# Kernel tuning notes

Measured on AMD Instinct MI355X. Metric: run time of the kernel, lower is better.

Reference implementation:

```python
import jax, jax.numpy as jnp
import numpy as np

B, L, HID = 4, 4096, 1024
H, D = 16, 64  # num_heads, head_dim


def setup_inputs() -> dict:
    key = jax.random.key(0)
    ks = jax.random.split(key, 5)
    s = 1.0 / np.sqrt(HID)
    mk = lambda k: jax.random.uniform(k, (HID, HID), minval=-s, maxval=s, dtype=jnp.float32)
    return {
        "x": jax.random.normal(ks[0], (B, L, HID), dtype=jnp.float32),
        "Wq": mk(ks[1]), "bq": jnp.zeros((HID,), jnp.float32),
        "Wk": mk(ks[2]), "bk": jnp.zeros((HID,), jnp.float32),
        "Wv": mk(ks[3]), "bv": jnp.zeros((HID,), jnp.float32),
        "Wo": mk(ks[4]), "bo": jnp.zeros((HID,), jnp.float32),
    }


def reference(x, Wq, bq, Wk, bk, Wv, bv, Wo, bo):
    Bx, Lx, _ = x.shape
    # projections (weights stored [in, out])
    q = (x @ Wq + bq).reshape(Bx, Lx, H, D)
    k = (x @ Wk + bk).reshape(Bx, Lx, H, D)
    v = (x @ Wv + bv).reshape(Bx, Lx, H, D)
    # Single window (L <= window_size): torch matmul batches over (B, L) and
    # contracts head_dim -> per-token head-to-head scores [B, L, H, H].
    scores = jnp.einsum('blhd,bled->blhe', q, k) / np.sqrt(D).astype(np.float32)
    probs = jax.nn.softmax(scores, axis=-1)
    out = jnp.einsum('blhe,bled->blhd', probs, v).reshape(Bx, Lx, HID)
    return out @ Wo + bo
```

## Files before the change

### kernel.cpp

```cpp
#include <hip/hip_runtime.h>
#include <stdint.h>


typedef __attribute__((ext_vector_type(8))) short short8;
typedef __attribute__((ext_vector_type(4))) float floatx4;
typedef __attribute__((address_space(1))) unsigned int gu32;
typedef __attribute__((address_space(3))) unsigned int lu32;

#define HID 1024
#define MTOK 16384
#define WELEM (HID * HID)
#define XELEM (MTOK * HID)

#define SBAR() __builtin_amdgcn_s_barrier()
#define WAITLGKM() do { asm volatile("s_waitcnt lgkmcnt(0)" ::: "memory"); \
                        __builtin_amdgcn_sched_barrier(0); } while (0)
#define VMCNT(n) do { asm volatile("s_waitcnt vmcnt(" #n ")" ::: "memory"); \
                      __builtin_amdgcn_sched_barrier(0); } while (0)

__device__ __forceinline__ unsigned short f2bf(float f) {
  union { float f; uint32_t u; } v; v.f = f;
  uint32_t u = v.u;
  u += 0x7fffu + ((u >> 16) & 1u);
  return (unsigned short)(u >> 16);
}

__global__ __launch_bounds__(256) void cvt_x_kernel(const float* __restrict__ x,
                                                    unsigned short* __restrict__ xb) {
  const int idx = blockIdx.x * 256 + threadIdx.x;
  float4 v = ((const float4*)x)[idx];
  ushort4 o;
  o.x = f2bf(v.x); o.y = f2bf(v.y); o.z = f2bf(v.z); o.w = f2bf(v.w);
  ((ushort4*)xb)[idx] = o;
}

__global__ __launch_bounds__(256) void cvt_w_kernel(const float* __restrict__ W0,
                                                    const float* __restrict__ W1,
                                                    const float* __restrict__ W2,
                                                    const float* __restrict__ W3,
                                                    unsigned short* __restrict__ WT) {
  const float* W = (blockIdx.z == 0) ? W0 : (blockIdx.z == 1) ? W1
                   : (blockIdx.z == 2) ? W2 : W3;
  unsigned short* out = WT + (size_t)blockIdx.z * WELEM;
  __shared__ float tile[64][65];
  const int t = threadIdx.x;
  const int n0 = blockIdx.x * 64, k0 = blockIdx.y * 64;
#pragma unroll
  for (int i = 0; i < 4; i++) {
    const int row = i * 16 + (t >> 4);
    const int col = (t & 15) * 4;
    float4 v = *(const float4*)&W[(size_t)(k0 + row) * HID + n0 + col];
    tile[row][col] = v.x; tile[row][col + 1] = v.y;
    tile[row][col + 2] = v.z; tile[row][col + 3] = v.w;
  }
  __syncthreads();
#pragma unroll
  for (int i = 0; i < 4; i++) {
    const int n = i * 16 + (t >> 4);
    const int k = (t & 15) * 4;
    ushort4 o;
    o.x = f2bf(tile[k][n]);     o.y = f2bf(tile[k + 1][n]);
    o.z = f2bf(tile[k + 2][n]); o.w = f2bf(tile[k + 3][n]);
    *(ushort4*)&out[(size_t)(n0 + n) * HID + k0 + k] = o;
  }
}

template <bool QKV>
__global__ __launch_bounds__(512, 2) void gemm256(
    const unsigned short* __restrict__ A,
    const unsigned short* __restrict__ BTb,
    const float* __restrict__ b0, const float* __restrict__ b1,
    const float* __restrict__ b2,
    void* __restrict__ Cv)
{
  __shared__ short8 smem_[131072 / 16];
  char* smem = (char*)smem_;

  constexpr int R = QKV ? 3 : 1;
  const int bid = blockIdx.x;
  const int xcd = bid & 7;
  const int j = bid >> 3;
  const int nb0 = j >> 3;
  const int mb = xcd * 8 + (j & 7);
  const int m0 = mb * 256;
  const int cb = nb0 * 256;

  const unsigned short* BT0 = QKV ? BTb : (BTb + (size_t)3 * WELEM);

  const int t_ = threadIdx.x;
  const int wv = t_ >> 6, lane = t_ & 63;
  const int quad = lane >> 4, r16 = lane & 15;
  const int wm = wv >> 2, wn = wv & 3;

  const int srow = wv * 16 + (lane >> 2);
  const int scol = ((lane & 3) ^ ((lane >> 3) & 3)) * 8;
  const unsigned short* Ag = A + (size_t)(m0 + srow) * HID + scol;
  const unsigned short* Bg = BT0 + (size_t)(cb + srow) * HID + scol;

  const int qsw = (quad ^ ((r16 >> 1) & 3)) << 4;
  const char* Ard = smem + wm * 16384 + r16 * 64 + qsw;
  const char* Brd = smem + 32768 + (wn >> 1) * 16384 + ((wn & 1) * 64 + r16) * 64 + qsw;

  floatx4 acc[8][4] = {};

  auto stageA = [&](int h, int tt) {
    const unsigned short* s = Ag + (size_t)h * 128 * HID + tt * 64;
    char* d = smem + ((tt & 1) << 16) + h * 16384 + wv * 1024;
    __builtin_amdgcn_global_load_lds((const gu32*)s,        (lu32*)d,          16, 0, 0);
    __builtin_amdgcn_global_load_lds((const gu32*)(s + 32), (lu32*)(d + 8192), 16, 0, 0);
  };
  auto stageB = [&](int h, int tt) {
    const unsigned short* s = Bg + (size_t)h * 128 * HID + tt * 64;
    char* d = smem + ((tt & 1) << 16) + 32768 + h * 16384 + wv * 1024;
    __builtin_amdgcn_global_load_lds((const gu32*)s,        (lu32*)d,          16, 0, 0);
    __builtin_amdgcn_global_load_lds((const gu32*)(s + 32), (lu32*)(d + 8192), 16, 0, 0);
  };

  const int NT = HID / 64;

  short8 alo[4][2], ahi[4][2];
  short8 b01[2][2], b23[2][2];

  stageA(0, 0); stageA(1, 0); stageB(0, 0); stageB(1, 0);
  VMCNT(0);
  SBAR();

  for (int r = 0; r < R; ++r) {
    for (int t = 0; t < NT; ++t) {
      const int bufb = (t & 1) << 16;
      const bool more = (t + 1 < NT);

      if (more) { stageA(0, t + 1); stageA(1, t + 1);
                  stageB(0, t + 1); stageB(1, t + 1); }

#pragma unroll
      for (int ks = 0; ks < 2; ++ks)
#pragma unroll
        for (int mi = 0; mi < 4; ++mi)
          alo[mi][ks] = *(const short8*)(Ard + bufb + ks * 8192 + mi * 1024);
#pragma unroll
      for (int ks = 0; ks < 2; ++ks)
#pragma unroll
        for (int ni = 0; ni < 2; ++ni)
          b01[ni][ks] = *(const short8*)(Brd + bufb + ks * 8192 + ni * 1024);
#pragma unroll
      for (int ks = 0; ks < 2; ++ks)
#pragma unroll
        for (int ni = 0; ni < 2; ++ni)
          b23[ni][ks] = *(const short8*)(Brd + bufb + ks * 8192 + (2 + ni) * 1024);
#pragma unroll
      for (int ks = 0; ks < 2; ++ks)
#pragma unroll
        for (int mi = 0; mi < 4; ++mi)
          ahi[mi][ks] = *(const short8*)(Ard + bufb + ks * 8192 + (4 + mi) * 1024);

      __builtin_amdgcn_s_setprio(1);
#pragma unroll
      for (int ks = 0; ks < 2; ++ks)
#pragma unroll
        for (int mi = 0; mi < 4; ++mi)
#pragma unroll
          for (int ni = 0; ni < 2; ++ni)
            acc[mi][ni] = __builtin_amdgcn_mfma_f32_16x16x32_bf16(alo[mi][ks], b01[ni][ks], acc[mi][ni], 0, 0, 0);
#pragma unroll
      for (int ks = 0; ks < 2; ++ks)
#pragma unroll
        for (int mi = 0; mi < 4; ++mi)
#pragma unroll
          for (int ni = 0; ni < 2; ++ni)
            acc[mi][2 + ni] = __builtin_amdgcn_mfma_f32_16x16x32_bf16(alo[mi][ks], b23[ni][ks], acc[mi][2 + ni], 0, 0, 0);
#pragma unroll
      for (int ks = 0; ks < 2; ++ks)
#pragma unroll
        for (int mi = 0; mi < 4; ++mi)
#pragma unroll
          for (int ni = 0; ni < 2; ++ni)
            acc[4 + mi][2 + ni] = __builtin_amdgcn_mfma_f32_16x16x32_bf16(ahi[mi][ks], b23[ni][ks], acc[4 + mi][2 + ni], 0, 0, 0);
#pragma unroll
      for (int ks = 0; ks < 2; ++ks)
#pragma unroll
        for (int mi = 0; mi < 4; ++mi)
#pragma unroll
          for (int ni = 0; ni < 2; ++ni)
            acc[4 + mi][ni] = __builtin_amdgcn_mfma_f32_16x16x32_bf16(ahi[mi][ks], b01[ni][ks], acc[4 + mi][ni], 0, 0, 0);
      __builtin_amdgcn_s_setprio(0);

      WAITLGKM();
      VMCNT(0);
      SBAR();
    }

    if (r + 1 < R) {
      Bg += WELEM;
      stageA(0, 0); stageA(1, 0); stageB(0, 0); stageB(1, 0);
    }

    {
      const float* bias = QKV ? ((r == 0) ? b0 : ((r == 1) ? b1 : b2)) : b0;
      float bvv[4];
#pragma unroll
      for (int ni = 0; ni < 4; ++ni) bvv[ni] = bias[cb + wn * 64 + ni * 16 + r16];

      const int row0 = m0 + wm * 128 + quad * 4;
      unsigned short* outb = (unsigned short*)Cv + (size_t)r * XELEM;
      float* outf = (float*)Cv;
#pragma unroll
      for (int mi = 0; mi < 8; ++mi) {
#pragma unroll
        for (int rr = 0; rr < 4; ++rr) {
          const size_t roff = (size_t)(row0 + mi * 16 + rr) * HID + cb + wn * 64 + r16;
#pragma unroll
          for (int ni = 0; ni < 4; ++ni) {
            const float val = acc[mi][ni][rr] + bvv[ni];
            if constexpr (QKV) outb[roff + ni * 16] = f2bf(val);
            else               outf[roff + ni * 16] = val;
          }
        }
      }
    }

    if (r + 1 < R) {
#pragma unroll
      for (int mi = 0; mi < 8; ++mi)
#pragma unroll
        for (int ni = 0; ni < 4; ++ni)
          acc[mi][ni] = floatx4{0.f, 0.f, 0.f, 0.f};
      VMCNT(0);
      SBAR();
    }
  }
}

__global__ __launch_bounds__(256) void attn_kernel(const unsigned short* qkv,
                                                   unsigned short* attn) {
  __shared__ unsigned short vls[4][1056];
  __shared__ unsigned short pls[4][16 * 24];

  const int t = threadIdx.x;
  const int wv = t >> 6, lane = t & 63;
  const int quad = lane >> 4, r16 = lane & 15;
  const size_t base = ((size_t)blockIdx.x * 4 + wv) * HID;
  const unsigned short* qp = qkv + base;
  const unsigned short* kp = qkv + (size_t)XELEM + base;
  const unsigned short* vp = qkv + 2 * (size_t)XELEM + base;

  __builtin_amdgcn_global_load_lds((const gu32*)(vp + lane * 8),       (lu32*)&vls[wv][0],   16, 0, 0);
  __builtin_amdgcn_global_load_lds((const gu32*)(vp + 512 + lane * 8), (lu32*)&vls[wv][528], 16, 0, 0);

  short8 qf0 = *(const short8*)(qp + r16 * 64 + quad * 8);
  short8 qf1 = *(const short8*)(qp + r16 * 64 + quad * 8 + 32);
  short8 kf0 = *(const short8*)(kp + r16 * 64 + quad * 8);
  short8 kf1 = *(const short8*)(kp + r16 * 64 + quad * 8 + 32);

  floatx4 sc = {0.f, 0.f, 0.f, 0.f};
  sc = __builtin_amdgcn_mfma_f32_16x16x32_bf16(qf0, kf0, sc, 0, 0, 0);
  sc = __builtin_amdgcn_mfma_f32_16x16x32_bf16(qf1, kf1, sc, 0, 0, 0);

#pragma unroll
  for (int rr = 0; rr < 4; rr++) {
    float s = sc[rr] * 0.125f;
    float m = s;
#pragma unroll
    for (int off = 1; off < 16; off <<= 1) m = fmaxf(m, __shfl_xor(m, off));
    float ex = __expf(s - m);
    float sum = ex;
#pragma unroll
    for (int off = 1; off < 16; off <<= 1) sum += __shfl_xor(sum, off);
    pls[wv][(quad * 4 + rr) * 24 + r16] = f2bf(ex / sum);
  }

  __syncthreads();

  const short8 zero8 = {0, 0, 0, 0, 0, 0, 0, 0};
  short8 af = zero8;
  short8 bf[4] = {zero8, zero8, zero8, zero8};
  if (quad < 2) {
    af = *(const short8*)&pls[wv][r16 * 24 + quad * 8];
#pragma unroll
    for (int c = 0; c < 4; c++)
#pragma unroll
      for (int jj = 0; jj < 8; jj++)
        bf[c][jj] = (short)vls[wv][quad * 528 + jj * 64 + c * 16 + r16];
  }

  floatx4 ov[4];
#pragma unroll
  for (int c = 0; c < 4; c++) {
    floatx4 z = {0.f, 0.f, 0.f, 0.f};
    ov[c] = __builtin_amdgcn_mfma_f32_16x16x32_bf16(af, bf[c], z, 0, 0, 0);
  }

#pragma unroll
  for (int rr = 0; rr < 4; rr++)
#pragma unroll
    for (int c = 0; c < 4; c++)
      attn[base + (size_t)(quad * 4 + rr) * 64 + c * 16 + r16] = f2bf(ov[c][rr]);
}

extern "C" void kernel_launch(void* const* d_in, const int* in_sizes, int n_in,
                              void* d_out, int out_size, void* d_ws, size_t ws_size,
                              hipStream_t stream) {
  const float* x  = (const float*)d_in[0];
  const float* Wq = (const float*)d_in[1];
  const float* bq = (const float*)d_in[2];
  const float* Wk = (const float*)d_in[3];
  const float* bk = (const float*)d_in[4];
  const float* Wv = (const float*)d_in[5];
  const float* bv = (const float*)d_in[6];
  const float* Wo = (const float*)d_in[7];
  const float* bo = (const float*)d_in[8];

  char* ws = (char*)d_ws;
  unsigned short* xb  = (unsigned short*)ws;
  unsigned short* wt  = (unsigned short*)(ws + (size_t)XELEM * 2);
  unsigned short* qkv = wt + 4 * (size_t)WELEM;

  cvt_x_kernel<<<XELEM / 1024, 256, 0, stream>>>(x, xb);
  cvt_w_kernel<<<dim3(16, 16, 4), 256, 0, stream>>>(Wq, Wk, Wv, Wo, wt);
  gemm256<true><<<256, 512, 0, stream>>>(xb, wt, bq, bk, bv, (void*)qkv);
  attn_kernel<<<4096, 256, 0, stream>>>(qkv, qkv);
  gemm256<false><<<256, 512, 0, stream>>>(qkv, wt, bo, bo, bo, d_out);
}
```

Measured before the change: 296.3 us.

## Switch GEMM to 32x32x16 MFMA with 4 waves and 128x128 warp tiles

Rewrites the 256x256 GEMM kernel to use 256 threads (4 waves), each computing a 128x128 sub-tile with 32x32x16 bf16 MFMAs instead of 8 waves using 16x16x32. Global-to-LDS staging now issues four loads per thread, and LDS fragment reads are double-buffered across k-substeps, interleaved with the MFMA groups. The aim is fewer LDS reads per FLOP and higher MFMA throughput per instruction. In exchange each wave holds many more accumulator registers, there is less wave-level parallelism to hide latency, and the setprio hints are gone.

```diff
diff --git a/kernel.cpp b/kernel.cpp
--- a/kernel.cpp
+++ b/kernel.cpp
@@ -4,6 +4,7 @@
 
 typedef __attribute__((ext_vector_type(8))) short short8;
 typedef __attribute__((ext_vector_type(4))) float floatx4;
+typedef __attribute__((ext_vector_type(16))) float floatx16;
 typedef __attribute__((address_space(1))) unsigned int gu32;
 typedef __attribute__((address_space(3))) unsigned int lu32;
 
@@ -66,7 +67,7 @@
 }
 
 template <bool QKV>
-__global__ __launch_bounds__(512, 2) void gemm256(
+__global__ __launch_bounds__(256, 1) void gemm256(
     const unsigned short* __restrict__ A,
     const unsigned short* __restrict__ BTb,
     const float* __restrict__ b0, const float* __restrict__ b1,
@@ -89,37 +90,65 @@
 
   const int t_ = threadIdx.x;
   const int wv = t_ >> 6, lane = t_ & 63;
-  const int quad = lane >> 4, r16 = lane & 15;
-  const int wm = wv >> 2, wn = wv & 3;
+  const int lm = lane & 31, lh = lane >> 5;
+  const int wm = wv >> 1, wn = wv & 1;
 
   const int srow = wv * 16 + (lane >> 2);
   const int scol = ((lane & 3) ^ ((lane >> 3) & 3)) * 8;
   const unsigned short* Ag = A + (size_t)(m0 + srow) * HID + scol;
   const unsigned short* Bg = BT0 + (size_t)(cb + srow) * HID + scol;
 
-  const int qsw = (quad ^ ((r16 >> 1) & 3)) << 4;
-  const char* Ard = smem + wm * 16384 + r16 * 64 + qsw;
-  const char* Brd = smem + 32768 + (wn >> 1) * 16384 + ((wn & 1) * 64 + r16) * 64 + qsw;
-
-  floatx4 acc[8][4] = {};
+  const int xr = (lm >> 1) & 3;
+  const int se = (lh ^ xr) << 4;
+  const int so = ((lh ^ xr) ^ 2) << 4;
+  const char* ArdW = smem + wm * 16384 + lm * 64;
+  const char* BrdW = smem + 32768 + wn * 16384 + lm * 64;
+
+  floatx16 acc[4][4];
+  const floatx16 z16 = {};
+#pragma unroll
+  for (int mi = 0; mi < 4; ++mi)
+#pragma unroll
+    for (int ni = 0; ni < 4; ++ni) acc[mi][ni] = z16;
 
   auto stageA = [&](int h, int tt) {
     const unsigned short* s = Ag + (size_t)h * 128 * HID + tt * 64;
     char* d = smem + ((tt & 1) << 16) + h * 16384 + wv * 1024;
-    __builtin_amdgcn_global_load_lds((const gu32*)s,        (lu32*)d,          16, 0, 0);
-    __builtin_amdgcn_global_load_lds((const gu32*)(s + 32), (lu32*)(d + 8192), 16, 0, 0);
+    __builtin_amdgcn_global_load_lds((const gu32*)s,                 (lu32*)d,                 16, 0, 0);
+    __builtin_amdgcn_global_load_lds((const gu32*)(s + 64 * HID),    (lu32*)(d + 4096),        16, 0, 0);
+    __builtin_amdgcn_global_load_lds((const gu32*)(s + 32),          (lu32*)(d + 8192),        16, 0, 0);
+    __builtin_amdgcn_global_load_lds((const gu32*)(s + 32 + 64*HID), (lu32*)(d + 8192 + 4096), 16, 0, 0);
   };
   auto stageB = [&](int h, int tt) {
     const unsigned short* s = Bg + (size_t)h * 128 * HID + tt * 64;
     char* d = smem + ((tt & 1) << 16) + 32768 + h * 16384 + wv * 1024;
-    __builtin_amdgcn_global_load_lds((const gu32*)s,        (lu32*)d,          16, 0, 0);
-    __builtin_amdgcn_global_load_lds((const gu32*)(s + 32), (lu32*)(d + 8192), 16, 0, 0);
+    __builtin_amdgcn_global_load_lds((const gu32*)s,                 (lu32*)d,                 16, 0, 0);
+    __builtin_amdgcn_global_load_lds((const gu32*)(s + 64 * HID),    (lu32*)(d + 4096),        16, 0, 0);
+    __builtin_amdgcn_global_load_lds((const gu32*)(s + 32),          (lu32*)(d + 8192),        16, 0, 0);
+    __builtin_amdgcn_global_load_lds((const gu32*)(s + 32 + 64*HID), (lu32*)(d + 8192 + 4096), 16, 0, 0);
   };
 
   const int NT = HID / 64;
 
-  short8 alo[4][2], ahi[4][2];
-  short8 b01[2][2], b23[2][2];
+  short8 aF[2][4], bF[2][4];
+
+  auto READ = [&](int p, int bufb, int ks) {
+    const int ko = (ks >> 1) * 8192 + ((ks & 1) ? so : se);
+#pragma unroll
+    for (int mi = 0; mi < 4; ++mi)
+      aF[p][mi] = *(const short8*)(ArdW + bufb + ko + mi * 2048);
+#pragma unroll
+    for (int ni = 0; ni < 4; ++ni)
+      bF[p][ni] = *(const short8*)(BrdW + bufb + ko + ni * 2048);
+  };
+  auto MM = [&](int p) {
+#pragma unroll
+    for (int mi = 0; mi < 4; ++mi)
+#pragma unroll
+      for (int ni = 0; ni < 4; ++ni)
+        acc[mi][ni] = __builtin_amdgcn_mfma_f32_32x32x16_bf16(
+            aF[p][mi], bF[p][ni], acc[mi][ni], 0, 0, 0);
+  };
 
   stageA(0, 0); stageA(1, 0); stageB(0, 0); stageB(1, 0);
   VMCNT(0);
@@ -133,57 +162,14 @@
       if (more) { stageA(0, t + 1); stageA(1, t + 1);
                   stageB(0, t + 1); stageB(1, t + 1); }
 
-#pragma unroll
-      for (int ks = 0; ks < 2; ++ks)
-#pragma unroll
-        for (int mi = 0; mi < 4; ++mi)
-          alo[mi][ks] = *(const short8*)(Ard + bufb + ks * 8192 + mi * 1024);
-#pragma unroll
-      for (int ks = 0; ks < 2; ++ks)
-#pragma unroll
-        for (int ni = 0; ni < 2; ++ni)
-          b01[ni][ks] = *(const short8*)(Brd + bufb + ks * 8192 + ni * 1024);
-#pragma unroll
-      for (int ks = 0; ks < 2; ++ks)
-#pragma unroll
-        for (int ni = 0; ni < 2; ++ni)
-          b23[ni][ks] = *(const short8*)(Brd + bufb + ks * 8192 + (2 + ni) * 1024);
-#pragma unroll
-      for (int ks = 0; ks < 2; ++ks)
-#pragma unroll
-        for (int mi = 0; mi < 4; ++mi)
-          ahi[mi][ks] = *(const short8*)(Ard + bufb + ks * 8192 + (4 + mi) * 1024);
-
-      __builtin_amdgcn_s_setprio(1);
-#pragma unroll
-      for (int ks = 0; ks < 2; ++ks)
-#pragma unroll
-        for (int mi = 0; mi < 4; ++mi)
-#pragma unroll
-          for (int ni = 0; ni < 2; ++ni)
-            acc[mi][ni] = __builtin_amdgcn_mfma_f32_16x16x32_bf16(alo[mi][ks], b01[ni][ks], acc[mi][ni], 0, 0, 0);
-#pragma unroll
-      for (int ks = 0; ks < 2; ++ks)
-#pragma unroll
-        for (int mi = 0; mi < 4; ++mi)
-#pragma unroll
-          for (int ni = 0; ni < 2; ++ni)
-            acc[mi][2 + ni] = __builtin_amdgcn_mfma_f32_16x16x32_bf16(alo[mi][ks], b23[ni][ks], acc[mi][2 + ni], 0, 0, 0);
-#pragma unroll
-      for (int ks = 0; ks < 2; ++ks)
-#pragma unroll
-        for (int mi = 0; mi < 4; ++mi)
-#pragma unroll
-          for (int ni = 0; ni < 2; ++ni)
-            acc[4 + mi][2 + ni] = __builtin_amdgcn_mfma_f32_16x16x32_bf16(ahi[mi][ks], b23[ni][ks], acc[4 + mi][2 + ni], 0, 0, 0);
-#pragma unroll
-      for (int ks = 0; ks < 2; ++ks)
-#pragma unroll
-        for (int mi = 0; mi < 4; ++mi)
-#pragma unroll
-          for (int ni = 0; ni < 2; ++ni)
-            acc[4 + mi][ni] = __builtin_amdgcn_mfma_f32_16x16x32_bf16(ahi[mi][ks], b01[ni][ks], acc[4 + mi][ni], 0, 0, 0);
-      __builtin_amdgcn_s_setprio(0);
+      READ(0, bufb, 0);
+      READ(1, bufb, 1);
+      MM(0);
+      READ(0, bufb, 2);
+      MM(1);
+      READ(1, bufb, 3);
+      MM(0);
+      MM(1);
 
       WAITLGKM();
       VMCNT(0);
@@ -199,21 +185,22 @@
       const float* bias = QKV ? ((r == 0) ? b0 : ((r == 1) ? b1 : b2)) : b0;
       float bvv[4];
 #pragma unroll
-      for (int ni = 0; ni < 4; ++ni) bvv[ni] = bias[cb + wn * 64 + ni * 16 + r16];
-
-      const int row0 = m0 + wm * 128 + quad * 4;
+      for (int ni = 0; ni < 4; ++ni) bvv[ni] = bias[cb + wn * 128 + ni * 32 + lm];
+
+      const int row0 = m0 + wm * 128 + 4 * lh;
       unsigned short* outb = (unsigned short*)Cv + (size_t)r * XELEM;
       float* outf = (float*)Cv;
 #pragma unroll
-      for (int mi = 0; mi < 8; ++mi) {
-#pragma unroll
-        for (int rr = 0; rr < 4; ++rr) {
-          const size_t roff = (size_t)(row0 + mi * 16 + rr) * HID + cb + wn * 64 + r16;
+      for (int mi = 0; mi < 4; ++mi) {
+#pragma unroll
+        for (int reg = 0; reg < 16; ++reg) {
+          const int row = row0 + mi * 32 + (reg & 3) + 8 * (reg >> 2);
+          const size_t roff = (size_t)row * HID + cb + wn * 128 + lm;
 #pragma unroll
           for (int ni = 0; ni < 4; ++ni) {
-            const float val = acc[mi][ni][rr] + bvv[ni];
-            if constexpr (QKV) outb[roff + ni * 16] = f2bf(val);
-            else               outf[roff + ni * 16] = val;
+            const float val = acc[mi][ni][reg] + bvv[ni];
+            if constexpr (QKV) outb[roff + ni * 32] = f2bf(val);
+            else               outf[roff + ni * 32] = val;
           }
         }
       }
@@ -221,10 +208,9 @@
 
     if (r + 1 < R) {
 #pragma unroll
-      for (int mi = 0; mi < 8; ++mi)
-#pragma unroll
-        for (int ni = 0; ni < 4; ++ni)
-          acc[mi][ni] = floatx4{0.f, 0.f, 0.f, 0.f};
+      for (int mi = 0; mi < 4; ++mi)
+#pragma unroll
+        for (int ni = 0; ni < 4; ++ni) acc[mi][ni] = z16;
       VMCNT(0);
       SBAR();
     }
@@ -317,7 +303,7 @@
 
   cvt_x_kernel<<<XELEM / 1024, 256, 0, stream>>>(x, xb);
   cvt_w_kernel<<<dim3(16, 16, 4), 256, 0, stream>>>(Wq, Wk, Wv, Wo, wt);
-  gemm256<true><<<256, 512, 0, stream>>>(xb, wt, bq, bk, bv, (void*)qkv);
+  gemm256<true><<<256, 256, 0, stream>>>(xb, wt, bq, bk, bv, (void*)qkv);
   attn_kernel<<<4096, 256, 0, stream>>>(qkv, qkv);
-  gemm256<false><<<256, 512, 0, stream>>>(qkv, wt, bo, bo, bo, d_out);
-}
+  gemm256<false><<<256, 256, 0, stream>>>(qkv, wt, bo, bo, bo, d_out);
+}
```

New measurement: 311.8 us. 1.05x slower.
